# Optimization experiments

Hardware: AMD Instinct MI355X
Metric: run time of the kernel (lower is better)

The kernel has to match this reference:

```python
import jax, jax.numpy as jnp
import numpy as np

NUM_HEADS = 16

def setup_inputs() -> dict:
    key = jax.random.key(0)
    ks = jax.random.split(key, 5)
    b, c, w, h = 2, 1024, 48, 48
    sc = 0.02
    return {
        "x": jax.random.normal(ks[0], (b, c, w, h), jnp.float32),
        "Wqkv": jax.random.normal(ks[1], (3 * c, c), jnp.float32) * sc,
        "bqkv": jax.random.normal(ks[2], (3 * c,), jnp.float32) * sc,
        "Wo": jax.random.normal(ks[3], (c, c), jnp.float32) * sc,
        "bo": jax.random.normal(ks[4], (c,), jnp.float32) * sc,
    }

def reference(x, Wqkv, bqkv, Wo, bo):
    b, c, w, h = x.shape
    n = NUM_HEADS
    hd = c // n
    s = w * h
    # [b,c,w,h] -> tokens [b, s, c]
    xs = x.transpose(0, 2, 3, 1).reshape(b, s, c)
    qkv = xs @ Wqkv.T + bqkv                       # [b, s, 3c]
    # rearrange 'b s (three n hd) -> three b n s hd'
    qkv = qkv.reshape(b, s, 3, n, hd).transpose(2, 0, 3, 1, 4)
    q, k, v = qkv[0], qkv[1], qkv[2]               # [b, n, s, hd]
    score = jnp.einsum('bnqh,bnkh->bnqk', q, k) / jnp.sqrt(jnp.float32(hd))
    # module uses a soft causal mask: subtract 10000 above the diagonal
    mask = 10000.0 * jnp.triu(jnp.ones((s, s), dtype=score.dtype), k=1)
    attn = jax.nn.softmax(score - mask, axis=-1)   # [b, n, s, s]
    z = jnp.einsum('bnqk,bnkh->bqnh', attn, v).reshape(b, s, c)
    out = z @ Wo.T + bo                            # [b, s, c]
    return out.reshape(b, w, h, c).transpose(0, 3, 1, 2)
```

## Files before the change

### kernel.cpp

```cpp
#include <hip/hip_runtime.h>

typedef __bf16 bf16;
typedef __bf16 bf16x8 __attribute__((ext_vector_type(8)));
typedef float floatx4 __attribute__((ext_vector_type(4)));
typedef float floatx16 __attribute__((ext_vector_type(16)));

static constexpr int S = 2304;
static constexpr int C = 1024;
static constexpr int NHEAD = 16;
static constexpr int HDIM = 64;
static constexpr int BATCH = 2;
static constexpr float QSCALE = 0.18033688011112042f;
static constexpr int QACC0 = 512;
static constexpr int NACCQ = S - QACC0;
static constexpr int NPART = 2;

__global__ __launch_bounds__(256) void k_convert(const float* __restrict__ src,
                                                 bf16* __restrict__ dst, int n8) {
  int i = blockIdx.x * 256 + threadIdx.x;
  if (i >= n8) return;
  float4 a = *(const float4*)(src + (size_t)i * 8);
  float4 b = *(const float4*)(src + (size_t)i * 8 + 4);
  bf16x8 o;
  o[0] = (bf16)a.x; o[1] = (bf16)a.y; o[2] = (bf16)a.z; o[3] = (bf16)a.w;
  o[4] = (bf16)b.x; o[5] = (bf16)b.y; o[6] = (bf16)b.z; o[7] = (bf16)b.w;
  *(bf16x8*)(dst + (size_t)i * 8) = o;
}

__global__ __launch_bounds__(256) void k_transpose(const float* __restrict__ x,
                                                   bf16* __restrict__ xs) {
  __shared__ bf16 T[64 * 72];
  int c0 = blockIdx.x * 64, t0 = blockIdx.y * 64, b = blockIdx.z;
  int tid = threadIdx.x;
  const float* xb = x + (size_t)b * C * S;
#pragma unroll
  for (int it = 0; it < 4; ++it) {
    int idx = it * 256 + tid;
    int rc = idx >> 4, t4 = idx & 15;
    float4 v = *(const float4*)(xb + (size_t)(c0 + rc) * S + t0 + t4 * 4);
    T[(t4 * 4 + 0) * 72 + rc] = (bf16)v.x;
    T[(t4 * 4 + 1) * 72 + rc] = (bf16)v.y;
    T[(t4 * 4 + 2) * 72 + rc] = (bf16)v.z;
    T[(t4 * 4 + 3) * 72 + rc] = (bf16)v.w;
  }
  __syncthreads();
  bf16* xsb = xs + (size_t)b * S * C;
#pragma unroll
  for (int it = 0; it < 2; ++it) {
    int idx = it * 256 + tid;
    int rt = idx >> 3, c8 = idx & 7;
    bf16x8 v;
#pragma unroll
    for (int i = 0; i < 8; ++i) v[i] = T[rt * 72 + c8 * 8 + i];
    *(bf16x8*)(xsb + (size_t)(t0 + rt) * C + c0 + c8 * 8) = v;
  }
}

__device__ __forceinline__ void g2l16(const bf16* g, bf16* l) {
  __builtin_amdgcn_global_load_lds(
      (const __attribute__((address_space(1))) void*)g,
      (__attribute__((address_space(3))) void*)l, 16, 0, 0);
}

__device__ __forceinline__ unsigned cvtpk(float a, float b) {
  unsigned r;
  asm("v_cvt_pk_bf16_f32 %0, %1, %2" : "=v"(r) : "v"(a), "v"(b));
  return r;
}

__device__ __forceinline__ void pl32(unsigned& a, unsigned& b) {
  asm("v_permlane32_swap_b32 %0, %1" : "+v"(a), "+v"(b));
}

template <int EPI>
__global__ __launch_bounds__(256) void k_gemm_bt(const bf16* __restrict__ A,
                                                 const bf16* __restrict__ Bt,
                                                 const float* __restrict__ bias,
                                                 bf16* __restrict__ q,
                                                 bf16* __restrict__ k,
                                                 bf16* __restrict__ v,
                                                 float* __restrict__ outf) {
  constexpr int K = C;
  __shared__ bf16 As[128 * 64];
  __shared__ bf16 Bs[128 * 64];
  int tid = threadIdx.x;
  int w = tid >> 6, lane = tid & 63, ln = lane & 15, quad = lane >> 4;
  int m0 = blockIdx.y * 128, n0 = blockIdx.x * 128;
  int moff = (w >> 1) * 64, noff = (w & 1) * 64;
  floatx4 acc[4][4] = {};

  int sr[4], sc[4];
#pragma unroll
  for (int it = 0; it < 4; ++it) {
    int L = (it * 4 + w) * 64 + lane;
    sr[it] = L >> 3;
    sc[it] = (L & 7) ^ (sr[it] & 7);
  }

  for (int k0 = 0; k0 < K; k0 += 64) {
    __syncthreads();
#pragma unroll
    for (int it = 0; it < 4; ++it) {
      int cb = (it * 4 + w) * 64;
      g2l16(A + (size_t)(m0 + sr[it]) * K + k0 + sc[it] * 8, As + cb * 8);
      g2l16(Bt + (size_t)(n0 + sr[it]) * K + k0 + sc[it] * 8, Bs + cb * 8);
    }
    __syncthreads();
#pragma unroll
    for (int t = 0; t < 2; ++t) {
      bf16x8 af[4], bfr[4];
#pragma unroll
      for (int i = 0; i < 4; ++i) {
        int ra = moff + i * 16 + ln;
        af[i]  = *(const bf16x8*)(As + ra * 64 + (((t * 4 + quad) ^ (ra & 7))) * 8);
        int rb = noff + i * 16 + ln;
        bfr[i] = *(const bf16x8*)(Bs + rb * 64 + (((t * 4 + quad) ^ (rb & 7))) * 8);
      }
#pragma unroll
      for (int im = 0; im < 4; ++im)
#pragma unroll
        for (int in = 0; in < 4; ++in)
          acc[im][in] = __builtin_amdgcn_mfma_f32_16x16x32_bf16(
              af[im], bfr[in], acc[im][in], 0, 0, 0);
    }
  }

  int bidx = (m0 >= S) ? 1 : 0;
  if (EPI == 0) {
#pragma unroll
    for (int in = 0; in < 4; ++in) {
      int j = n0 + noff + in * 16 + ln;
      float bv = bias[j];
      int three = j >> 10;
      int head = (j >> 6) & 15;
      int hdi = j & 63;
#pragma unroll
      for (int im = 0; im < 4; ++im) {
        int mbase = m0 + moff + im * 16 + quad * 4;
        int tb = mbase - bidx * S;
        if (three == 2) {
          union { ushort4 u; bf16 h[4]; } P;
#pragma unroll
          for (int r = 0; r < 4; ++r) P.h[r] = (bf16)(acc[im][in][r] + bv);
          *(ushort4*)(v + ((size_t)(bidx * NHEAD + head) * HDIM + hdi) * S + tb) = P.u;
        } else if (three == 0) {
          bf16* dst = q + ((size_t)(bidx * NHEAD + head) * S + tb) * HDIM + hdi;
#pragma unroll
          for (int r = 0; r < 4; ++r)
            dst[(size_t)r * HDIM] = (bf16)((acc[im][in][r] + bv) * QSCALE);
        } else {
          bf16* dst = k + ((size_t)(bidx * NHEAD + head) * S + tb) * HDIM + hdi;
#pragma unroll
          for (int r = 0; r < 4; ++r) dst[(size_t)r * HDIM] = (bf16)(acc[im][in][r] + bv);
        }
      }
    }
  } else {
#pragma unroll
    for (int in = 0; in < 4; ++in) {
      int co = n0 + noff + in * 16 + ln;
      float bv = bias[co];
#pragma unroll
      for (int im = 0; im < 4; ++im) {
        int mbase = m0 + moff + im * 16 + quad * 4;
        int tb = mbase - bidx * S;
        float4 st;
        st.x = acc[im][in][0] + bv;
        st.y = acc[im][in][1] + bv;
        st.z = acc[im][in][2] + bv;
        st.w = acc[im][in][3] + bv;
        *(float4*)(outf + ((size_t)bidx * C + co) * S + tb) = st;
      }
    }
  }
}

__global__ __launch_bounds__(512) void k_attn_part(const bf16* __restrict__ Qg,
                                                   const bf16* __restrict__ Kg,
                                                   const bf16* __restrict__ Vtg,
                                                   bf16* __restrict__ z,
                                                   float* __restrict__ Oacc,
                                                   float* __restrict__ Lacc) {
  __shared__ bf16 Ks[2][64 * 64];
  __shared__ bf16 Vs[2][64 * 64];
  static const unsigned char QT[16] = {8,8,7,7,6,6,5,5,4,4,1,3,3,2,2,0};
  static const unsigned char LO[16] = {0,18,0,16,0,14,0,12,0,10,0,0,8,0,6,0};
  static const unsigned char HI[16] = {18,36,16,32,14,28,12,24,10,20,8,8,16,6,12,4};
  static const unsigned char PT[16] = {0,1,0,1,0,1,0,1,0,1,0,0,1,0,1,0};
  int i = blockIdx.x;
  int xcd = i & 7, j = i >> 3;
  int grp = j >> 4, r = j & 15;
  int bh = xcd + 8 * grp;
  int qt = QT[r], lo = LO[r], hi = HI[r], part = PT[r];
  bool single = (qt <= 1);
  int b = bh >> 4, h = bh & 15;
  int tid = threadIdx.x;
  int w = tid >> 6, lane = tid & 63;
  int ql = lane & 31, hw = lane >> 5;
  int qw = qt * 256 + w * 32;
  int qg = qw + ql;
  int ktd = qw >> 6;

  const bf16* kb = Kg + (size_t)bh * S * HDIM;
  const bf16* vb = Vtg + (size_t)bh * HDIM * S;

  int s_row = tid >> 3;
  int s_c8 = (tid & 7) ^ (s_row & 7);
  size_t kOff = (size_t)s_row * HDIM + s_c8 * 8;
  size_t vOff = (size_t)s_row * S + s_c8 * 8;

  const bf16* qb = Qg + ((size_t)bh * S + qg) * HDIM + hw * 8;
  bf16x8 qf[4];
#pragma unroll
  for (int c = 0; c < 4; ++c) qf[c] = *(const bf16x8*)(qb + c * 16);

  float lsA = 0.f, lsB = 0.f;
  floatx16 o0 = {}, o1 = {};

  const bf16* kb0 = kb + (size_t)lo * 64 * HDIM;
  const bf16* vb0 = vb + (size_t)lo * 64;
  g2l16(kb0 + kOff, Ks[0] + tid * 8);
  g2l16(vb0 + vOff, Vs[0] + tid * 8);

  const bf16* kbn = kb0 + (size_t)64 * HDIM;
  const bf16* vbn = vb0 + 64;

  int qsw = ql & 7;

#pragma unroll 1
  for (int kt = lo; kt < hi; ++kt) {
    int cur = (kt - lo) & 1;
    __syncthreads();

    if (kt + 1 < hi) {
      g2l16(kbn + kOff, Ks[1 - cur] + tid * 8);
      g2l16(vbn + vOff, Vs[1 - cur] + tid * 8);
      kbn += (size_t)64 * HDIM;
      vbn += 64;
    }

    if (kt > ktd) continue;
    bool diag = (kt == ktd);

    const bf16* ksb = Ks[cur];
    const bf16* vsb = Vs[cur];

    floatx16 sa0 = {}, sa1 = {};
    __builtin_amdgcn_s_setprio(1);
#pragma unroll
    for (int c = 0; c < 4; ++c) {
      int c8 = ((2 * c + hw) ^ qsw) * 8;
      bf16x8 k0 = *(const bf16x8*)(ksb + ql * 64 + c8);
      bf16x8 k1 = *(const bf16x8*)(ksb + (32 + ql) * 64 + c8);
      sa0 = __builtin_amdgcn_mfma_f32_32x32x16_bf16(k0, qf[c], sa0, 0, 0, 0);
      sa1 = __builtin_amdgcn_mfma_f32_32x32x16_bf16(k1, qf[c], sa1, 0, 0, 0);
    }
    __builtin_amdgcn_s_setprio(0);

    unsigned pk0[8], pk1[8];
    if (!diag) {
#pragma unroll
      for (int t = 0; t < 8; ++t) {
        float a = exp2f(sa0[2 * t]), c2 = exp2f(sa0[2 * t + 1]);
        float d = exp2f(sa1[2 * t]), e = exp2f(sa1[2 * t + 1]);
        lsA += a + c2;
        lsB += d + e;
        pk0[t] = cvtpk(a, c2);
        pk1[t] = cvtpk(d, e);
      }
    } else {
      int qd = qg - kt * 64;
#pragma unroll
      for (int t = 0; t < 8; ++t) {
        int r0 = 2 * t, r1 = 2 * t + 1;
        int k0l = (r0 & 3) + 8 * (r0 >> 2) + 4 * hw;
        int k1l = (r1 & 3) + 8 * (r1 >> 2) + 4 * hw;
        float a = (k0l > qd) ? 0.f : exp2f(sa0[r0]);
        float c2 = (k1l > qd) ? 0.f : exp2f(sa0[r1]);
        float d = (32 + k0l > qd) ? 0.f : exp2f(sa1[r0]);
        float e = (32 + k1l > qd) ? 0.f : exp2f(sa1[r1]);
        lsA += a + c2;
        lsB += d + e;
        pk0[t] = cvtpk(a, c2);
        pk1[t] = cvtpk(d, e);
      }
    }

    __builtin_amdgcn_s_setprio(1);
#pragma unroll
    for (int ktc = 0; ktc < 4; ++ktc) {
      unsigned d0, d1, d2, d3;
      if (ktc == 0)      { d0 = pk0[0]; d1 = pk0[1]; d2 = pk0[2]; d3 = pk0[3]; }
      else if (ktc == 1) { d0 = pk0[4]; d1 = pk0[5]; d2 = pk0[6]; d3 = pk0[7]; }
      else if (ktc == 2) { d0 = pk1[0]; d1 = pk1[1]; d2 = pk1[2]; d3 = pk1[3]; }
      else               { d0 = pk1[4]; d1 = pk1[5]; d2 = pk1[6]; d3 = pk1[7]; }
      pl32(d0, d2);
      pl32(d1, d3);
      union { unsigned u[4]; bf16x8 v; } pf;
      pf.u[0] = d0; pf.u[1] = d1; pf.u[2] = d2; pf.u[3] = d3;
      int c8 = ((2 * ktc + hw) ^ qsw) * 8;
      bf16x8 v0 = *(const bf16x8*)(vsb + ql * 64 + c8);
      bf16x8 v1 = *(const bf16x8*)(vsb + (32 + ql) * 64 + c8);
      o0 = __builtin_amdgcn_mfma_f32_32x32x16_bf16(v0, pf.v, o0, 0, 0, 0);
      o1 = __builtin_amdgcn_mfma_f32_32x32x16_bf16(v1, pf.v, o1, 0, 0, 0);
    }
    __builtin_amdgcn_s_setprio(0);
  }

  float lsum = lsA + lsB;
  lsum += __shfl_xor(lsum, 32);

  if (single) {
    float inv = 1.f / lsum;
    bf16* dst = z + ((size_t)b * S + qg) * C + h * HDIM + 4 * hw;
#pragma unroll
    for (int hdblk = 0; hdblk < 2; ++hdblk) {
#pragma unroll
      for (int rg = 0; rg < 4; ++rg) {
        union { ushort4 u; bf16 hh[4]; } P;
#pragma unroll
        for (int jj = 0; jj < 4; ++jj) {
          float ov = hdblk ? o1[rg * 4 + jj] : o0[rg * 4 + jj];
          P.hh[jj] = (bf16)(ov * inv);
        }
        *(ushort4*)(dst + hdblk * 32 + rg * 8) = P.u;
      }
    }
  } else {
    int qa = qg - QACC0;
    float* ob = Oacc + (((size_t)part * 32 + bh) * NACCQ + qa) * 64;
    if (hw == 0) Lacc[((size_t)part * 32 + bh) * NACCQ + qa] = lsum;
#pragma unroll
    for (int g = 0; g < 4; ++g) {
      *(float4*)(ob + 4 * hw + 8 * g) =
          float4{o0[4 * g], o0[4 * g + 1], o0[4 * g + 2], o0[4 * g + 3]};
      *(float4*)(ob + 32 + 4 * hw + 8 * g) =
          float4{o1[4 * g], o1[4 * g + 1], o1[4 * g + 2], o1[4 * g + 3]};
    }
  }
}

__global__ __launch_bounds__(256) void k_norm(const float* __restrict__ Oacc,
                                              const float* __restrict__ Lacc,
                                              bf16* __restrict__ z) {
  int qt = blockIdx.x, bh = blockIdx.y;
  int b = bh >> 4, h = bh & 15;
  int tid = threadIdx.x;
  int q = tid >> 2;
  int seg = tid & 3;
  int qa = qt * 64 + q;
  float l = Lacc[(size_t)bh * NACCQ + qa] +
            Lacc[((size_t)32 + bh) * NACCQ + qa];
  float inv = 1.f / l;
  const float* o0 = Oacc + ((size_t)bh * NACCQ + qa) * 64 + seg * 16;
  const float* o1 = Oacc + (((size_t)32 + bh) * NACCQ + qa) * 64 + seg * 16;
  bf16* dst = z + ((size_t)b * S + QACC0 + qa) * C + h * HDIM + seg * 16;
#pragma unroll
  for (int half = 0; half < 2; ++half) {
    float4 a0 = *(const float4*)(o0 + half * 8);
    float4 a1 = *(const float4*)(o0 + half * 8 + 4);
    float4 b0 = *(const float4*)(o1 + half * 8);
    float4 b1 = *(const float4*)(o1 + half * 8 + 4);
    bf16x8 o;
    o[0] = (bf16)((a0.x + b0.x) * inv);
    o[1] = (bf16)((a0.y + b0.y) * inv);
    o[2] = (bf16)((a0.z + b0.z) * inv);
    o[3] = (bf16)((a0.w + b0.w) * inv);
    o[4] = (bf16)((a1.x + b1.x) * inv);
    o[5] = (bf16)((a1.y + b1.y) * inv);
    o[6] = (bf16)((a1.z + b1.z) * inv);
    o[7] = (bf16)((a1.w + b1.w) * inv);
    *(bf16x8*)(dst + half * 8) = o;
  }
}

extern "C" void kernel_launch(void* const* d_in, const int* in_sizes, int n_in,
                              void* d_out, int out_size, void* d_ws, size_t ws_size,
                              hipStream_t stream) {
  const float* x    = (const float*)d_in[0];
  const float* Wqkv = (const float*)d_in[1];
  const float* bqkv = (const float*)d_in[2];
  const float* Wo   = (const float*)d_in[3];
  const float* bo   = (const float*)d_in[4];
  float* out = (float*)d_out;

  bf16* ws = (bf16*)d_ws;
  const size_t tok = (size_t)BATCH * S * C;
  bf16* xs   = ws;
  bf16* Qg   = ws + tok;
  bf16* Kg   = ws + 2 * tok;
  bf16* Vtg  = ws + 3 * tok;
  bf16* Wqb  = ws + 4 * tok;
  bf16* Wob  = Wqb + (size_t)3 * C * C;
  float* Oacc = (float*)(Wob + (size_t)C * C);
  float* Lacc = Oacc + (size_t)NPART * 32 * NACCQ * 64;
  bf16* z    = xs;

  k_convert<<<(3 * C * C / 8 + 255) / 256, 256, 0, stream>>>(Wqkv, Wqb, 3 * C * C / 8);
  k_convert<<<(C * C / 8 + 255) / 256, 256, 0, stream>>>(Wo, Wob, C * C / 8);
  k_transpose<<<dim3(C / 64, S / 64, BATCH), 256, 0, stream>>>(x, xs);
  k_gemm_bt<0><<<dim3(3 * C / 128, BATCH * S / 128), 256, 0, stream>>>(
      xs, Wqb, bqkv, Qg, Kg, Vtg, nullptr);
  k_attn_part<<<dim3(512), 512, 0, stream>>>(Qg, Kg, Vtg, z, Oacc, Lacc);
  k_norm<<<dim3(28, 32), 256, 0, stream>>>(Oacc, Lacc, z);
  k_gemm_bt<1><<<dim3(C / 128, BATCH * S / 128), 256, 0, stream>>>(
      z, Wob, bo, nullptr, nullptr, nullptr, out);
}
```

Before: 223.1 us.

## Split long causal attention rows into three KV partitions with triple-buffered loads

New measurement: 221.3 us. Within noise of the previous version (-0.8%).

```diff
diff --git a/kernel.cpp b/kernel.cpp
--- a/kernel.cpp
+++ b/kernel.cpp
@@ -13,7 +13,7 @@
 static constexpr float QSCALE = 0.18033688011112042f;
 static constexpr int QACC0 = 512;
 static constexpr int NACCQ = S - QACC0;
-static constexpr int NPART = 2;
+static constexpr int NPART = 3;
 
 __global__ __launch_bounds__(256) void k_convert(const float* __restrict__ src,
                                                  bf16* __restrict__ dst, int n8) {
@@ -181,15 +181,15 @@
                                                    bf16* __restrict__ z,
                                                    float* __restrict__ Oacc,
                                                    float* __restrict__ Lacc) {
-  __shared__ bf16 Ks[2][64 * 64];
-  __shared__ bf16 Vs[2][64 * 64];
-  static const unsigned char QT[16] = {8,8,7,7,6,6,5,5,4,4,1,3,3,2,2,0};
-  static const unsigned char LO[16] = {0,18,0,16,0,14,0,12,0,10,0,0,8,0,6,0};
-  static const unsigned char HI[16] = {18,36,16,32,14,28,12,24,10,20,8,8,16,6,12,4};
-  static const unsigned char PT[16] = {0,1,0,1,0,1,0,1,0,1,0,0,1,0,1,0};
+  __shared__ bf16 Ks[3][64 * 64];
+  __shared__ bf16 Vs[3][64 * 64];
+  static const unsigned char QT[22] = {8,8,8,7,7,7,6,6,6,5,5,5,1,4,4,4,3,2,2,3,3,0};
+  static const unsigned char LO[22] = {0,12,24,0,11,22,0,10,19,0,8,16,0,0,7,14,0,0,6,6,11,0};
+  static const unsigned char HI[22] = {12,24,36,11,22,32,10,19,28,8,16,24,8,7,14,20,6,6,12,11,16,4};
+  static const unsigned char PT[22] = {0,1,2,0,1,2,0,1,2,0,1,2,0,0,1,2,0,0,1,1,2,0};
   int i = blockIdx.x;
   int xcd = i & 7, j = i >> 3;
-  int grp = j >> 4, r = j & 15;
+  int grp = j / 22, r = j % 22;
   int bh = xcd + 8 * grp;
   int qt = QT[r], lo = LO[r], hi = HI[r], part = PT[r];
   bool single = (qt <= 1);
@@ -226,24 +226,28 @@
   const bf16* vbn = vb0 + 64;
 
   int qsw = ql & 7;
+  int cur = 0;
 
 #pragma unroll 1
   for (int kt = lo; kt < hi; ++kt) {
-    int cur = (kt - lo) & 1;
-    __syncthreads();
-
+    int nxt = (cur == 2) ? 0 : cur + 1;
     if (kt + 1 < hi) {
-      g2l16(kbn + kOff, Ks[1 - cur] + tid * 8);
-      g2l16(vbn + vOff, Vs[1 - cur] + tid * 8);
+      g2l16(kbn + kOff, Ks[nxt] + tid * 8);
+      g2l16(vbn + vOff, Vs[nxt] + tid * 8);
       kbn += (size_t)64 * HDIM;
       vbn += 64;
-    }
+      asm volatile("s_waitcnt vmcnt(2)" ::: "memory");
+    } else {
+      asm volatile("s_waitcnt vmcnt(0)" ::: "memory");
+    }
+    __builtin_amdgcn_s_barrier();
+
+    const bf16* ksb = Ks[cur];
+    const bf16* vsb = Vs[cur];
+    cur = nxt;
 
     if (kt > ktd) continue;
     bool diag = (kt == ktd);
-
-    const bf16* ksb = Ks[cur];
-    const bf16* vsb = Vs[cur];
 
     floatx16 sa0 = {}, sa1 = {};
     __builtin_amdgcn_s_setprio(1);
@@ -349,11 +353,14 @@
   int q = tid >> 2;
   int seg = tid & 3;
   int qa = qt * 64 + q;
+  bool np3 = (qa >= 256);
   float l = Lacc[(size_t)bh * NACCQ + qa] +
             Lacc[((size_t)32 + bh) * NACCQ + qa];
+  if (np3) l += Lacc[((size_t)64 + bh) * NACCQ + qa];
   float inv = 1.f / l;
   const float* o0 = Oacc + ((size_t)bh * NACCQ + qa) * 64 + seg * 16;
   const float* o1 = Oacc + (((size_t)32 + bh) * NACCQ + qa) * 64 + seg * 16;
+  const float* o2 = Oacc + (((size_t)64 + bh) * NACCQ + qa) * 64 + seg * 16;
   bf16* dst = z + ((size_t)b * S + QACC0 + qa) * C + h * HDIM + seg * 16;
 #pragma unroll
   for (int half = 0; half < 2; ++half) {
@@ -361,15 +368,23 @@
     float4 a1 = *(const float4*)(o0 + half * 8 + 4);
     float4 b0 = *(const float4*)(o1 + half * 8);
     float4 b1 = *(const float4*)(o1 + half * 8 + 4);
+    float s0 = a0.x + b0.x, s1 = a0.y + b0.y, s2 = a0.z + b0.z, s3 = a0.w + b0.w;
+    float s4 = a1.x + b1.x, s5 = a1.y + b1.y, s6 = a1.z + b1.z, s7 = a1.w + b1.w;
+    if (np3) {
+      float4 c0 = *(const float4*)(o2 + half * 8);
+      float4 c1 = *(const float4*)(o2 + half * 8 + 4);
+      s0 += c0.x; s1 += c0.y; s2 += c0.z; s3 += c0.w;
+      s4 += c1.x; s5 += c1.y; s6 += c1.z; s7 += c1.w;
+    }
     bf16x8 o;
-    o[0] = (bf16)((a0.x + b0.x) * inv);
-    o[1] = (bf16)((a0.y + b0.y) * inv);
-    o[2] = (bf16)((a0.z + b0.z) * inv);
-    o[3] = (bf16)((a0.w + b0.w) * inv);
-    o[4] = (bf16)((a1.x + b1.x) * inv);
-    o[5] = (bf16)((a1.y + b1.y) * inv);
-    o[6] = (bf16)((a1.z + b1.z) * inv);
-    o[7] = (bf16)((a1.w + b1.w) * inv);
+    o[0] = (bf16)(s0 * inv);
+    o[1] = (bf16)(s1 * inv);
+    o[2] = (bf16)(s2 * inv);
+    o[3] = (bf16)(s3 * inv);
+    o[4] = (bf16)(s4 * inv);
+    o[5] = (bf16)(s5 * inv);
+    o[6] = (bf16)(s6 * inv);
+    o[7] = (bf16)(s7 * inv);
     *(bf16x8*)(dst + half * 8) = o;
   }
 }
@@ -401,7 +416,7 @@
   k_transpose<<<dim3(C / 64, S / 64, BATCH), 256, 0, stream>>>(x, xs);
   k_gemm_bt<0><<<dim3(3 * C / 128, BATCH * S / 128), 256, 0, stream>>>(
       xs, Wqb, bqkv, Qg, Kg, Vtg, nullptr);
-  k_attn_part<<<dim3(512), 512, 0, stream>>>(Qg, Kg, Vtg, z, Oacc, Lacc);
+  k_attn_part<<<dim3(704), 512, 0, stream>>>(Qg, Kg, Vtg, z, Oacc, Lacc);
   k_norm<<<dim3(28, 32), 256, 0, stream>>>(Oacc, Lacc, z);
   k_gemm_bt<1><<<dim3(C / 128, BATCH * S / 128), 256, 0, stream>>>(
       z, Wob, bo, nullptr, nullptr, nullptr, out);
```
